# Optimization experiments

Hardware: AMD Instinct MI355X
Metric: run time of the kernel (lower is better)

Reference implementation:

```python
import jax, jax.numpy as jnp
import numpy as np

T, N, C, L, H, NA, NL = 32, 64, 64, 64, 256, 16, 128


def _gru_dir(x, wi, wh, bi, bh):
    # x: [Lt, N, H] time-major; PyTorch GRU gate order (r, z, n). Returns [Lt, N, H].
    xi = jnp.einsum('tnh,gh->tng', x, wi) + bi  # precompute input projections [Lt,N,3H]
    def step(h, gi):
        gh = h @ wh.T + bh
        ir, iz, inn = jnp.split(gi, 3, -1)
        hr, hz, hn = jnp.split(gh, 3, -1)
        r = jax.nn.sigmoid(ir + hr)
        z = jax.nn.sigmoid(iz + hz)
        n = jnp.tanh(inn + r * hn)
        hnew = (1.0 - z) * n + z * h
        return hnew, hnew
    h0 = jnp.zeros((x.shape[1], wh.shape[1]), x.dtype)
    _, ys = jax.lax.scan(step, h0, xi)
    return ys


def setup_inputs() -> dict:
    key = jax.random.key(0)
    ks = jax.random.split(key, 32)
    s = 0.05
    p = {}
    p['condition'] = jax.random.normal(ks[0], (T, N, C), jnp.float32)
    p['lines'] = jax.random.randint(ks[1], (N, L), 0, NL)
    p['a_idx'] = jax.random.randint(ks[2], (T, N), 0, NA)
    p['p_idx'] = jax.random.randint(ks[3], (T, N), 0, L)
    p['embed'] = jax.random.normal(ks[4], (NL, H)) * s
    p['aemb'] = jax.random.normal(ks[5], (NA, H)) * s
    p['gru_wi_f'] = jax.random.normal(ks[6], (3 * H, H)) * s
    p['gru_wh_f'] = jax.random.normal(ks[7], (3 * H, H)) * s
    p['gru_bi_f'] = jax.random.normal(ks[8], (3 * H,)) * s
    p['gru_bh_f'] = jax.random.normal(ks[9], (3 * H,)) * s
    p['gru_wi_b'] = jax.random.normal(ks[10], (3 * H, H)) * s
    p['gru_wh_b'] = jax.random.normal(ks[11], (3 * H, H)) * s
    p['gru_bi_b'] = jax.random.normal(ks[12], (3 * H,)) * s
    p['gru_bh_b'] = jax.random.normal(ks[13], (3 * H,)) * s
    p['f_w1'] = jax.random.normal(ks[14], (H, C + H)) * s
    p['f_b1'] = jax.random.normal(ks[15], (H,)) * s
    p['f_w2'] = jax.random.normal(ks[16], (H, H)) * s
    p['f_b2'] = jax.random.normal(ks[17], (H,)) * s
    p['cell_wi'] = jax.random.normal(ks[18], (3 * H, H)) * s
    p['cell_wh'] = jax.random.normal(ks[19], (3 * H, H)) * s
    p['cell_bi'] = jax.random.normal(ks[20], (3 * H,)) * s
    p['cell_bh'] = jax.random.normal(ks[21], (3 * H,)) * s
    p['critic_w'] = jax.random.normal(ks[22], (1, H)) * s
    p['critic_b'] = jax.random.normal(ks[23], (1,)) * s
    p['pointer_w'] = jax.random.normal(ks[24], (L, H)) * s
    p['pointer_b'] = jax.random.normal(ks[25], (L,)) * s
    p['actor_w'] = jax.random.normal(ks[26], (NA, H)) * s
    p['actor_b'] = jax.random.normal(ks[27], (NA,)) * s
    p['query_w'] = jax.random.normal(ks[28], (H, H)) * s
    p['query_b'] = jax.random.normal(ks[29], (H,)) * s
    return p


def reference(condition, lines, a_idx, p_idx, embed, aemb,
              gru_wi_f, gru_wh_f, gru_bi_f, gru_bh_f,
              gru_wi_b, gru_wh_b, gru_bi_b, gru_bh_b,
              f_w1, f_b1, f_w2, f_b2,
              cell_wi, cell_wh, cell_bi, cell_bh,
              critic_w, critic_b, pointer_w, pointer_b,
              actor_w, actor_b, query_w, query_b):
    Tn, Nn = a_idx.shape
    Ln = lines.shape[1]
    Hd = embed.shape[1]
    M = embed[lines]                           # [N,L,H]
    x = jnp.transpose(M, (1, 0, 2))            # [L,N,H] time-major
    # torch.roll(x, shifts=i): rolled[i, j] = x[(j - i) % L]
    idx = (jnp.arange(Ln)[None, :] - jnp.arange(Ln)[:, None]) % Ln
    rolled = x[idx]                            # [L_roll, L_time, N, H]
    def bigru(seq):
        f = _gru_dir(seq, gru_wi_f, gru_wh_f, gru_bi_f, gru_bh_f)
        b = _gru_dir(seq[::-1], gru_wi_b, gru_wh_b, gru_bi_b, gru_bh_b)[::-1]
        return jnp.concatenate([f, b], -1)     # [L_time,N,2H]
    K1 = jax.vmap(bigru)(rolled)               # [L,L,N,2H]
    K = K1.reshape(Ln, Ln, Nn, 2, Hd).transpose(2, 0, 1, 3, 4).reshape(Nn, Ln, 2 * Ln, Hd)
    # A[t-1] for t=0 is hx.a == 0 (fresh episode, zero hidden state)
    a_prev = jnp.concatenate([jnp.zeros((1, Nn), a_idx.dtype), a_idx[:-1]], 0)
    rng_n = jnp.arange(Nn)
    def step(h, inp):
        cond_t, ap_t, p_t, a_t = inp
        obs = jnp.concatenate([cond_t, aemb[ap_t]], -1)
        xf = jax.nn.relu(obs @ f_w1.T + f_b1)
        xf = jax.nn.relu(xf @ f_w2.T + f_b2)
        gi = xf @ cell_wi.T + cell_bi
        gh = h @ cell_wh.T + cell_bh
        ir, iz, inn = jnp.split(gi, 3, -1)
        hr, hz, hn = jnp.split(gh, 3, -1)
        r = jax.nn.sigmoid(ir + hr)
        z = jax.nn.sigmoid(iz + hz)
        n = jnp.tanh(inn + r * hn)
        h = (1.0 - z) * n + z * h
        p_probs = jax.nn.softmax(h @ pointer_w.T + pointer_b, -1)
        q = h @ query_w.T + query_b
        k = K[rng_n, p_t]                      # gather: [N, 2L, H]
        l = jnp.einsum('nkh,nh->nk', k, q)
        zz = jnp.einsum('nk,nkh->nh', l, k)
        a_probs = jax.nn.softmax(zz @ actor_w.T + actor_b, -1)
        v = h @ critic_w.T + critic_b
        out = jnp.concatenate([a_t[:, None].astype(h.dtype), p_t[:, None].astype(h.dtype),
                               v, h, a_probs, p_probs], -1)
        return h, out
    h0 = jnp.zeros((Nn, Hd), condition.dtype)
    _, hxs = jax.lax.scan(step, h0, (condition, a_prev, p_idx, a_idx))
    return hxs  # packed RecurrentState: [T, N, 1+1+1+H+na+L]
```

## Files before the change

### kernel.cpp

```cpp
#include <hip/hip_runtime.h>
#include <hip/hip_bf16.h>
#include <cstddef>
#include <cstdint>

typedef __bf16 bf16;
typedef bf16 bf16x8 __attribute__((ext_vector_type(8)));
typedef float f32x4 __attribute__((ext_vector_type(4)));

#define DEV static __device__ __forceinline__

DEV f32x4 mfma_bf16(bf16x8 a, bf16x8 b, f32x4 c) {
  return __builtin_amdgcn_mfma_f32_16x16x32_bf16(a, b, c, 0, 0, 0);
}
DEV f32x4 mfma_fp8(long a, long b, f32x4 c) {
  return __builtin_amdgcn_mfma_f32_16x16x32_fp8_fp8(a, b, c, 0, 0, 0);
}

DEV float sigmoid_f(float x) { return 1.0f / (1.0f + __expf(-x)); }
DEV float tanh_f(float x) {
  float ax = fabsf(x);
  float e = __expf(-2.0f * ax);
  float t = 1.0f - 2.0f * e / (1.0f + e);
  return copysignf(t, x);
}
DEV unsigned char fp8_of(float x) {
  return (unsigned char)(__builtin_amdgcn_cvt_pk_fp8_f32(x, x, 0, false) & 0xFF);
}

static constexpr int H_ = 256;

static constexpr int o_embed = 0;
static constexpr int o_aemb = 32768;
static constexpr int o_wi_f = 36864;
static constexpr int o_wh_f = 233472;
static constexpr int o_bi_f = 430080;
static constexpr int o_bh_f = 430848;
static constexpr int o_wi_b = 431616;
static constexpr int o_wh_b = 628224;
static constexpr int o_bi_b = 824832;
static constexpr int o_bh_b = 825600;
static constexpr int o_f_w1 = 826368;
static constexpr int o_f_b1 = 908288;
static constexpr int o_f_w2 = 908544;
static constexpr int o_f_b2 = 974080;
static constexpr int o_cell_wi = 974336;
static constexpr int o_cell_wh = 1170944;
static constexpr int o_cell_bi = 1367552;
static constexpr int o_cell_bh = 1368320;
static constexpr int o_critic_w = 1369088;
static constexpr int o_critic_b = 1369344;
static constexpr int o_pointer_w = 1369360;
static constexpr int o_pointer_b = 1385744;
static constexpr int o_actor_w = 1385808;
static constexpr int o_actor_b = 1389904;
static constexpr int o_query_w = 1389920;
static constexpr int o_query_b = 1455456;
static constexpr int CW_TOTAL = 1455712;
static constexpr int WH8_TOTAL = 393216;
static constexpr int PREP_TOTAL = CW_TOTAL + WH8_TOTAL;
static constexpr int PREP_WGS = (PREP_TOTAL + 2047) / 2048;

static constexpr size_t XI_OFF = 0;
static constexpr size_t XI_BYTES = 2ull * 4096 * 768 * 2;
static constexpr size_t K1_OFF = XI_OFF + XI_BYTES;
static constexpr size_t K1_BYTES = 64ull * 32 * 128 * 256;
static constexpr size_t GI_OFF = K1_OFF + K1_BYTES;
static constexpr size_t GI_BYTES = 32ull * 64 * 768 * 4;
static constexpr size_t HD_OFF = GI_OFF + GI_BYTES;
static constexpr size_t HD_BYTES = 32ull * 64 * 256 * 4;
static constexpr size_t SLOT_OFF = HD_OFF + HD_BYTES;
static constexpr size_t SLOT_BYTES = 64ull * 64 * 4;
static constexpr size_t FLG_OFF = SLOT_OFF + SLOT_BYTES;
static constexpr size_t FLG_BYTES = 256;
static constexpr size_t WL_OFF = FLG_OFF + FLG_BYTES;
static constexpr size_t WL_BYTES = 8448;
static constexpr size_t CW_OFF = WL_OFF + WL_BYTES;
static constexpr size_t CW_BYTES = (size_t)CW_TOTAL * 2;
static constexpr size_t WH8_OFF = ((CW_OFF + CW_BYTES + 255) / 256) * 256;

static constexpr int XI_DIR_BYTES = 4096 * 768 * 2;
static constexpr int XI_U_BYTES = 64 * 768 * 2;

struct PrepArgs {
  const void* src[26];
  int off[26];
  int cnt[26];
};

__global__ __launch_bounds__(256)
void k_prep(PrepArgs pa, const uint32_t* __restrict__ cond, const uint32_t* __restrict__ emb,
            const void* __restrict__ whf_src, const void* __restrict__ whb_src,
            const int* __restrict__ p_idx, int* __restrict__ flags,
            bf16* __restrict__ cw, unsigned char* __restrict__ wh8,
            int* __restrict__ slot_map, int* __restrict__ wl) {
  int bx = blockIdx.x;
  int tid = threadIdx.x;
  __shared__ int votes[256];

  int c1 = 0;
  {
    uint32_t w0 = emb[tid * 2], w1 = emb[tid * 2 + 1];
    int e0 = (int)((w0 >> 7) & 0xFF), e1 = (int)((w1 >> 7) & 0xFF);
    c1 += (e0 >= 96 && e0 <= 130) ? 1 : 0;
    c1 += (e1 >= 96 && e1 <= 130) ? 1 : 0;
  }
  votes[tid] = c1;
  __syncthreads();
  __shared__ int f32w_s;
  if (tid == 0) {
    int s = 0;
    for (int i = 0; i < 256; i++) s += votes[i];
    f32w_s = (s < 256) ? 1 : 0;
  }
  __syncthreads();
  bool f32w = f32w_s != 0;

  if (bx == 0) {
    __syncthreads();
    int c0 = 0;
    {
      uint32_t w0 = cond[tid * 2], w1 = cond[tid * 2 + 1];
      int e0 = (int)((w0 >> 7) & 0xFF), e1 = (int)((w1 >> 7) & 0xFF);
      c0 += (e0 >= 96 && e0 <= 130) ? 1 : 0;
      c0 += (e1 >= 96 && e1 <= 130) ? 1 : 0;
    }
    votes[tid] = c0;
    __syncthreads();
    if (tid == 0) {
      int s = 0;
      for (int i = 0; i < 256; i++) s += votes[i];
      flags[0] = (s < 256) ? 1 : 0;
      flags[1] = f32w ? 1 : 0;
    }
  }

  if (bx < PREP_WGS) {
    int gidx = bx * 2048 + tid;
    for (int e = 0; e < 8; e++, gidx += 256) {
      if (gidx >= PREP_TOTAL) break;
      if (gidx < CW_TOTAL) {
        int rem = gidx, s = 0;
        while (s < 26 && rem >= pa.cnt[s]) { rem -= pa.cnt[s]; s++; }
        if (s < 26) {
          float v = f32w ? ((const float*)pa.src[s])[rem]
                         : (float)((const bf16*)pa.src[s])[rem];
          cw[pa.off[s] + rem] = (bf16)v;
        }
      } else {
        int i = gidx - CW_TOTAL;
        const void* src = (i < 196608) ? whf_src : whb_src;
        int k = (i < 196608) ? i : i - 196608;
        float v = f32w ? ((const float*)src)[k] : (float)((const bf16*)src)[k];
        wh8[i] = fp8_of(v);
      }
    }
    return;
  }

  __shared__ int pbuf[2048];
  __shared__ signed char sm[4096];
  __shared__ unsigned short entL[8 * 512];
  __shared__ int cntL[8];
  for (int i = tid; i < 2048; i += 256) pbuf[i] = p_idx[i];
  for (int i = tid; i < 4096; i += 256) sm[i] = -1;
  __syncthreads();
  if (tid < 64) {
    int n = tid, cnt = 0;
    for (int t = 0; t < 32; t++) {
      int p = pbuf[t * 64 + n];
      if (sm[n * 64 + p] < 0) sm[n * 64 + p] = (signed char)(cnt++);
    }
  }
  __syncthreads();
  for (int i = tid; i < 4096; i += 256) slot_map[i] = (int)sm[i];
  if (tid < 8) {
    int xcd = tid, cnt = 0;
    for (int roll = xcd * 8; roll < xcd * 8 + 8; roll++)
      for (int n = 0; n < 64; n++)
        if (sm[n * 64 + roll] >= 0) entL[xcd * 512 + (cnt++)] = (unsigned short)(n | (roll << 8));
    unsigned short pad = (unsigned short)((xcd * 8) << 8);
    while (cnt & 15) entL[xcd * 512 + (cnt++)] = pad;
    cntL[xcd] = cnt;
  }
  __syncthreads();
  if (tid < 8) wl[tid] = cntL[tid] >> 4;
  unsigned short* we = (unsigned short*)((char*)wl + 64);
  for (int i = tid; i < 8 * 512; i += 256) we[i] = entL[i];
}

__global__ __launch_bounds__(256)
void k_xi_gi(const int* __restrict__ lines, const bf16* __restrict__ cw,
             const void* __restrict__ cond_raw, const int* __restrict__ flags,
             const int* __restrict__ a_idx, bf16* __restrict__ xi,
             float* __restrict__ gi) {
  int bx = blockIdx.x;
  int tid = threadIdx.x;
  int w = tid >> 6, l = tid & 63, quad = l >> 4, l15 = l & 15;
  __shared__ __attribute__((aligned(16))) bf16 s_a[32 * 328];
  __shared__ __attribute__((aligned(16))) bf16 s_b[32 * 264];

  if (bx < 256) {
    int dir = bx & 1, rb = bx >> 1;
    const bf16* embed = cw + o_embed;
    const bf16* wi = cw + (dir ? o_wi_b : o_wi_f);
    const bf16* bi = cw + (dir ? o_bi_b : o_bi_f);
    bf16* xs = s_a;
    {
      int row = tid >> 3, seg = tid & 7;
      int grow = rb * 32 + row;
      int u = grow >> 6, n = grow & 63;
      int line = lines[n * 64 + u];
      const bf16* src = embed + (size_t)line * H_ + seg * 32;
      bf16* dst = xs + row * 264 + seg * 32;
#pragma unroll
      for (int e = 0; e < 4; e++) *(bf16x8*)(dst + e * 8) = *(const bf16x8*)(src + e * 8);
    }
    __syncthreads();
    f32x4 acc[2][12];
#pragma unroll
    for (int mt = 0; mt < 2; mt++)
#pragma unroll
      for (int nt = 0; nt < 12; nt++) acc[mt][nt] = f32x4{0.f, 0.f, 0.f, 0.f};
#pragma unroll
    for (int ks = 0; ks < 8; ks++) {
      int koff = ks * 32 + quad * 8;
      bf16x8 a0 = *(const bf16x8*)(xs + l15 * 264 + koff);
      bf16x8 a1 = *(const bf16x8*)(xs + (l15 + 16) * 264 + koff);
#pragma unroll
      for (int nt = 0; nt < 12; nt++) {
        int g = (w * 12 + nt) * 16 + l15;
        bf16x8 b = *(const bf16x8*)(wi + (size_t)g * H_ + koff);
        acc[0][nt] = mfma_bf16(a0, b, acc[0][nt]);
        acc[1][nt] = mfma_bf16(a1, b, acc[1][nt]);
      }
    }
    size_t base = (size_t)dir * 4096 * 768;
#pragma unroll
    for (int nt = 0; nt < 12; nt++) {
      int g = (w * 12 + nt) * 16 + l15;
      float bias = (float)bi[g];
#pragma unroll
      for (int mt = 0; mt < 2; mt++)
#pragma unroll
        for (int r = 0; r < 4; r++) {
          int m = mt * 16 + quad * 4 + r;
          xi[base + (size_t)(rb * 32 + m) * 768 + g] = (bf16)(acc[mt][nt][r] + bias);
        }
    }
    return;
  }

  int rb = bx - 256;
  const bf16* aemb = cw + o_aemb;
  const bf16* f_w1 = cw + o_f_w1;
  const bf16* f_b1 = cw + o_f_b1;
  const bf16* f_w2 = cw + o_f_w2;
  const bf16* f_b2 = cw + o_f_b2;
  const bf16* cell_wi = cw + o_cell_wi;
  const bf16* cell_bi = cw + o_cell_bi;
  bool cf32 = flags[0] != 0;
  bf16* obs = s_a;
  bf16* xf1 = s_b;

  for (int e = tid; e < 32 * 320; e += 256) {
    int row = e / 320, col = e - row * 320;
    int grow = rb * 32 + row;
    int t = grow >> 6, n = grow & 63;
    float v;
    if (col < 64) {
      v = cf32 ? ((const float*)cond_raw)[(size_t)grow * 64 + col]
               : (float)((const bf16*)cond_raw)[(size_t)grow * 64 + col];
    } else {
      int ap = (t == 0) ? 0 : a_idx[(t - 1) * 64 + n];
      v = (float)aemb[ap * 256 + (col - 64)];
    }
    obs[row * 328 + col] = (bf16)v;
  }
  __syncthreads();
  {
    f32x4 acc[2][4];
#pragma unroll
    for (int mt = 0; mt < 2; mt++)
#pragma unroll
      for (int nt = 0; nt < 4; nt++) acc[mt][nt] = f32x4{0.f, 0.f, 0.f, 0.f};
#pragma unroll
    for (int ks = 0; ks < 10; ks++) {
      int koff = ks * 32 + quad * 8;
      bf16x8 a0 = *(const bf16x8*)(obs + l15 * 328 + koff);
      bf16x8 a1 = *(const bf16x8*)(obs + (l15 + 16) * 328 + koff);
#pragma unroll
      for (int nt = 0; nt < 4; nt++) {
        int g = (w * 4 + nt) * 16 + l15;
        bf16x8 b = *(const bf16x8*)(f_w1 + (size_t)g * 320 + koff);
        acc[0][nt] = mfma_bf16(a0, b, acc[0][nt]);
        acc[1][nt] = mfma_bf16(a1, b, acc[1][nt]);
      }
    }
#pragma unroll
    for (int nt = 0; nt < 4; nt++) {
      int g = (w * 4 + nt) * 16 + l15;
      float bias = (float)f_b1[g];
#pragma unroll
      for (int mt = 0; mt < 2; mt++)
#pragma unroll
        for (int r = 0; r < 4; r++) {
          int m = mt * 16 + quad * 4 + r;
          xf1[m * 264 + g] = (bf16)fmaxf(acc[mt][nt][r] + bias, 0.f);
        }
    }
  }
  __syncthreads();
  bf16* xf2 = obs;
  {
    f32x4 acc[2][4];
#pragma unroll
    for (int mt = 0; mt < 2; mt++)
#pragma unroll
      for (int nt = 0; nt < 4; nt++) acc[mt][nt] = f32x4{0.f, 0.f, 0.f, 0.f};
#pragma unroll
    for (int ks = 0; ks < 8; ks++) {
      int koff = ks * 32 + quad * 8;
      bf16x8 a0 = *(const bf16x8*)(xf1 + l15 * 264 + koff);
      bf16x8 a1 = *(const bf16x8*)(xf1 + (l15 + 16) * 264 + koff);
#pragma unroll
      for (int nt = 0; nt < 4; nt++) {
        int g = (w * 4 + nt) * 16 + l15;
        bf16x8 b = *(const bf16x8*)(f_w2 + (size_t)g * 256 + koff);
        acc[0][nt] = mfma_bf16(a0, b, acc[0][nt]);
        acc[1][nt] = mfma_bf16(a1, b, acc[1][nt]);
      }
    }
#pragma unroll
    for (int nt = 0; nt < 4; nt++) {
      int g = (w * 4 + nt) * 16 + l15;
      float bias = (float)f_b2[g];
#pragma unroll
      for (int mt = 0; mt < 2; mt++)
#pragma unroll
        for (int r = 0; r < 4; r++) {
          int m = mt * 16 + quad * 4 + r;
          xf2[m * 264 + g] = (bf16)fmaxf(acc[mt][nt][r] + bias, 0.f);
        }
    }
  }
  __syncthreads();
  {
    f32x4 acc[2][12];
#pragma unroll
    for (int mt = 0; mt < 2; mt++)
#pragma unroll
      for (int nt = 0; nt < 12; nt++) acc[mt][nt] = f32x4{0.f, 0.f, 0.f, 0.f};
#pragma unroll
    for (int ks = 0; ks < 8; ks++) {
      int koff = ks * 32 + quad * 8;
      bf16x8 a0 = *(const bf16x8*)(xf2 + l15 * 264 + koff);
      bf16x8 a1 = *(const bf16x8*)(xf2 + (l15 + 16) * 264 + koff);
#pragma unroll
      for (int nt = 0; nt < 12; nt++) {
        int g = (w * 12 + nt) * 16 + l15;
        bf16x8 b = *(const bf16x8*)(cell_wi + (size_t)g * 256 + koff);
        acc[0][nt] = mfma_bf16(a0, b, acc[0][nt]);
        acc[1][nt] = mfma_bf16(a1, b, acc[1][nt]);
      }
    }
#pragma unroll
    for (int nt = 0; nt < 12; nt++) {
      int g = (w * 12 + nt) * 16 + l15;
      float bias = (float)cell_bi[g];
#pragma unroll
      for (int mt = 0; mt < 2; mt++)
#pragma unroll
        for (int r = 0; r < 4; r++) {
          int m = mt * 16 + quad * 4 + r;
          gi[(size_t)(rb * 32 + m) * 768 + g] = acc[mt][nt][r] + bias;
        }
    }
  }
}

__global__ __launch_bounds__(1024, 4)
void k_main(const bf16* __restrict__ cw, const unsigned char* __restrict__ wh8,
            const bf16* __restrict__ xi, const int* __restrict__ slot_map,
            const int* __restrict__ wl, const float* __restrict__ gi,
            unsigned char* __restrict__ K1c, float* __restrict__ hdec) {
  int bx = blockIdx.x;
  int tid = threadIdx.x;
  int w = tid >> 6, l = tid & 63, quad = l >> 4, l15 = l & 15;
  int c = w * 16 + l15;
  __shared__ __attribute__((aligned(16))) unsigned char smem[2][16 * 264 * 2];

  if (bx < 512) {
    int xcd = bx & 7, dir = (bx >> 3) & 1, slot = bx >> 4;
    if (slot >= wl[xcd]) return;
    const unsigned short* we = (const unsigned short*)((const char*)wl + 64) + xcd * 512 + slot * 16;
    const unsigned char* whd = wh8 + (size_t)dir * 196608;
    const bf16* bh = cw + (dir ? o_bh_b : o_bh_f);

    unsigned char (*hb)[16 * 264 * 2] = smem;
    for (int idx = tid; idx < 16 * 264; idx += 1024) hb[0][idx] = 0;

    long bfr[3][8];
#pragma unroll
    for (int g = 0; g < 3; g++) {
      const unsigned char* bp = whd + (size_t)(g * 256 + c) * 256 + quad * 8;
#pragma unroll
      for (int ks = 0; ks < 8; ks++) bfr[g][ks] = *(const long*)(bp + ks * 32);
    }

    int xoff[4];
    uint32_t slice[4];
    bool valid[4];
#pragma unroll
    for (int r = 0; r < 4; r++) {
      int e = we[quad * 4 + r];
      int roll = e >> 8, n = e & 255;
      int u0 = dir ? ((63 - roll) & 63) : ((64 - roll) & 63);
      xoff[r] = u0 * XI_U_BYTES + n * 1536 + c * 2;
      int ks = slot_map[n * 64 + roll];
      valid[r] = ks >= 0;
      slice[r] = (uint32_t)((n * 32 + (ks < 0 ? 0 : ks)) * 32768);
    }
    int ustep = dir ? -XI_U_BYTES : XI_U_BYTES;
    int jbase = dir ? (63 * 2 + 1) * 256 : 0;
    int jstep = dir ? -512 : 512;

    float hreg[4] = {0.f, 0.f, 0.f, 0.f};
    float bhv[3];
#pragma unroll
    for (int g = 0; g < 3; g++) bhv[g] = (float)bh[g * 256 + c];

    const char* xid = (const char*)xi + (size_t)dir * XI_DIR_BYTES;
    __syncthreads();

    int cur = 0;
    for (int t = 0; t < 64; t++) {
      float xiv[3][4];
#pragma unroll
      for (int r = 0; r < 4; r++) {
        const bf16* xp = (const bf16*)(xid + xoff[r]);
        xiv[0][r] = (float)xp[0];
        xiv[1][r] = (float)xp[256];
        xiv[2][r] = (float)xp[512];
        xoff[r] += ustep;
        if (xoff[r] >= XI_DIR_BYTES) xoff[r] -= XI_DIR_BYTES;
        if (xoff[r] < 0) xoff[r] += XI_DIR_BYTES;
      }

      f32x4 accA[3], accB[3];
#pragma unroll
      for (int g = 0; g < 3; g++) {
        accA[g] = f32x4{0.f, 0.f, 0.f, 0.f};
        accB[g] = f32x4{0.f, 0.f, 0.f, 0.f};
      }
#pragma unroll
      for (int ks = 0; ks < 4; ks++) {
        long a0 = *(const long*)(hb[cur] + l15 * 264 + ks * 32 + quad * 8);
        long a1 = *(const long*)(hb[cur] + l15 * 264 + (ks + 4) * 32 + quad * 8);
#pragma unroll
        for (int g = 0; g < 3; g++) {
          accA[g] = mfma_fp8(a0, bfr[g][ks], accA[g]);
          accB[g] = mfma_fp8(a1, bfr[g][ks + 4], accB[g]);
        }
      }

      int nxt = cur ^ 1;
#pragma unroll
      for (int r = 0; r < 4; r++) {
        float rg = sigmoid_f(xiv[0][r] + accA[0][r] + accB[0][r] + bhv[0]);
        float zg = sigmoid_f(xiv[1][r] + accA[1][r] + accB[1][r] + bhv[1]);
        float ng = tanh_f(xiv[2][r] + rg * (accA[2][r] + accB[2][r] + bhv[2]));
        hreg[r] = (1.f - zg) * ng + zg * hreg[r];
        unsigned char hb8 = fp8_of(hreg[r]);
        hb[nxt][(quad * 4 + r) * 264 + c] = hb8;
        if (valid[r]) K1c[(size_t)slice[r] + jbase + c] = hb8;
      }
      jbase += jstep;
      __syncthreads();
      cur = nxt;
    }
    return;
  }

  int nq = bx - 512;
  const bf16* wh = cw + o_cell_wh;
  const bf16* bh = cw + o_cell_bh;
  bf16 (*hb)[16 * 264] = (bf16(*)[16 * 264])smem;
  for (int idx = tid; idx < 16 * 264; idx += 1024) hb[0][idx] = (bf16)0.f;

  float hreg[4] = {0.f, 0.f, 0.f, 0.f};
  float bhv[3];
  const bf16* bp[3];
#pragma unroll
  for (int g = 0; g < 3; g++) {
    int grow = g * 256 + c;
    bhv[g] = (float)bh[grow];
    bp[g] = wh + (size_t)grow * 256 + quad * 8;
  }
  __syncthreads();

  int cur = 0;
  for (int t = 0; t < 32; t++) {
    const float* gr = gi + ((size_t)t * 64 + nq * 16) * 768;
    float giv[3][4];
#pragma unroll
    for (int r = 0; r < 4; r++)
#pragma unroll
      for (int g = 0; g < 3; g++)
        giv[g][r] = gr[(quad * 4 + r) * 768 + g * 256 + c];

    f32x4 acc[3];
#pragma unroll
    for (int g = 0; g < 3; g++) acc[g] = f32x4{0.f, 0.f, 0.f, 0.f};
#pragma unroll
    for (int ks = 0; ks < 8; ks++) {
      int ko = ks * 32 + quad * 8;
      bf16x8 a0 = *(const bf16x8*)(hb[cur] + l15 * 264 + ko);
#pragma unroll
      for (int g = 0; g < 3; g++) {
        bf16x8 b = *(const bf16x8*)(bp[g] + ks * 32);
        acc[g] = mfma_bf16(a0, b, acc[g]);
      }
    }
    int nxt = cur ^ 1;
#pragma unroll
    for (int r = 0; r < 4; r++) {
      float rg = sigmoid_f(giv[0][r] + acc[0][r] + bhv[0]);
      float zg = sigmoid_f(giv[1][r] + acc[1][r] + bhv[1]);
      float ng = tanh_f(giv[2][r] + rg * (acc[2][r] + bhv[2]));
      float hnew = (1.f - zg) * ng + zg * hreg[r];
      hreg[r] = hnew;
      hb[nxt][(quad * 4 + r) * 264 + c] = (bf16)hnew;
      hdec[((size_t)t * 64 + nq * 16 + quad * 4 + r) * 256 + c] = hnew;
    }
    __syncthreads();
    cur = nxt;
  }
}

__global__ __launch_bounds__(256)
void k_post(const float* __restrict__ hdec, const unsigned char* __restrict__ K1c,
            const int* __restrict__ slot_map, const int* __restrict__ flags,
            const int* __restrict__ a_idx, const int* __restrict__ p_idx,
            const bf16* __restrict__ cw, void* __restrict__ out_raw) {
  int bx = blockIdx.x;
  int tid = threadIdx.x;
  int w = tid >> 6, l = tid & 63, quad = l >> 4, l15 = l & 15;
  __shared__ __attribute__((aligned(16))) unsigned char sraw[38032];
  bool f32o = flags[1] != 0;

  if (bx < 64) {
    int rb = bx;
    const bf16* pointer_w = cw + o_pointer_w;
    const bf16* pointer_b = cw + o_pointer_b;
    const bf16* critic_w = cw + o_critic_w;
    const bf16* critic_b = cw + o_critic_b;
    bf16* hsb = (bf16*)sraw;
    float* pls = (float*)(sraw + 16896);
    float* vred = (float*)(sraw + 16896 + 8448);

    for (int idx = tid; idx < 32 * 256; idx += 256) {
      int row = idx >> 8, col = idx & 255;
      hsb[row * 264 + col] = (bf16)hdec[(size_t)(rb * 32 + row) * 256 + col];
    }
    __syncthreads();

    {
      f32x4 acc[2];
      acc[0] = f32x4{0.f, 0.f, 0.f, 0.f};
      acc[1] = f32x4{0.f, 0.f, 0.f, 0.f};
      int g = w * 16 + l15;
#pragma unroll
      for (int ks = 0; ks < 8; ks++) {
        int koff = ks * 32 + quad * 8;
        bf16x8 a0 = *(const bf16x8*)(hsb + l15 * 264 + koff);
        bf16x8 a1 = *(const bf16x8*)(hsb + (l15 + 16) * 264 + koff);
        bf16x8 b = *(const bf16x8*)(pointer_w + (size_t)g * 256 + koff);
        acc[0] = mfma_bf16(a0, b, acc[0]);
        acc[1] = mfma_bf16(a1, b, acc[1]);
      }
      float bias = (float)pointer_b[g];
#pragma unroll
      for (int mt = 0; mt < 2; mt++)
#pragma unroll
        for (int r = 0; r < 4; r++) {
          int m = mt * 16 + quad * 4 + r;
          pls[m * 66 + g] = acc[mt][r] + bias;
        }
    }
    {
      int row = tid >> 3, seg = tid & 7;
      float acc = 0.f;
#pragma unroll
      for (int k = 0; k < 32; k++)
        acc += (float)hsb[row * 264 + seg * 32 + k] * (float)critic_w[seg * 32 + k];
      vred[row * 8 + seg] = acc;
    }
    __syncthreads();

    if (tid < 32) {
      float mx = -1e30f;
      for (int k = 0; k < 64; k++) mx = fmaxf(mx, pls[tid * 66 + k]);
      float sm = 0.f;
      for (int k = 0; k < 64; k++) {
        float e = __expf(pls[tid * 66 + k] - mx);
        pls[tid * 66 + k] = e;
        sm += e;
      }
      float inv = 1.f / sm;
      for (int k = 0; k < 64; k++) pls[tid * 66 + k] *= inv;
      float v = (float)critic_b[0];
      for (int s = 0; s < 8; s++) v += vred[tid * 8 + s];
      vred[tid * 8] = v;
    }
    __syncthreads();

    if (f32o) {
      float* ob = (float*)out_raw;
      if (tid < 32) {
        int grow = rb * 32 + tid;
        ob[(size_t)grow * 339 + 0] = (float)a_idx[grow];
        ob[(size_t)grow * 339 + 1] = (float)p_idx[grow];
        ob[(size_t)grow * 339 + 2] = vred[tid * 8];
      }
      for (int idx = tid; idx < 32 * 256; idx += 256) {
        int row = idx >> 8, col = idx & 255;
        int grow = rb * 32 + row;
        ob[(size_t)grow * 339 + 3 + col] = hdec[(size_t)grow * 256 + col];
      }
      for (int idx = tid; idx < 32 * 64; idx += 256) {
        int row = idx >> 6, col = idx & 63;
        ob[(size_t)(rb * 32 + row) * 339 + 275 + col] = pls[row * 66 + col];
      }
    } else {
      bf16* ob = (bf16*)out_raw;
      if (tid < 32) {
        int grow = rb * 32 + tid;
        ob[(size_t)grow * 339 + 0] = (bf16)(float)a_idx[grow];
        ob[(size_t)grow * 339 + 1] = (bf16)(float)p_idx[grow];
        ob[(size_t)grow * 339 + 2] = (bf16)vred[tid * 8];
      }
      for (int idx = tid; idx < 32 * 256; idx += 256) {
        int row = idx >> 8, col = idx & 255;
        int grow = rb * 32 + row;
        ob[(size_t)grow * 339 + 3 + col] = (bf16)hdec[(size_t)grow * 256 + col];
      }
      for (int idx = tid; idx < 32 * 64; idx += 256) {
        int row = idx >> 6, col = idx & 63;
        ob[(size_t)(rb * 32 + row) * 339 + 275 + col] = (bf16)pls[row * 66 + col];
      }
    }
    return;
  }

  int tn = bx - 64;
  int t = tn >> 6, n = tn & 63;
  const bf16* actor_w = cw + o_actor_w;
  const bf16* actor_b = cw + o_actor_b;
  const bf16* query_w = cw + o_query_w;
  const bf16* query_b = cw + o_query_b;

  unsigned char* ksb = sraw;
  float* hs = (float*)(sraw + 33792);
  float* qs = (float*)(sraw + 33792 + 1024);
  float* ls = (float*)(sraw + 33792 + 2048);
  float* sA = (float*)(sraw + 33792 + 3072);
  float* al = (float*)(sraw + 33792 + 4096);

  hs[tid] = hdec[((size_t)t * 64 + n) * 256 + tid];
  int p = p_idx[t * 64 + n];
  int slot = slot_map[n * 64 + p];
  {
    const uint32_t* kg = (const uint32_t*)(K1c + ((size_t)n * 32 + slot) * 32768);
#pragma unroll
    for (int e = 0; e < 8; e++) {
      int flat = (e * 256 + tid) * 16;
      int kk = flat >> 8, col = flat & 255;
      uint32_t w0 = kg[(flat >> 2) + 0], w1 = kg[(flat >> 2) + 1];
      uint32_t w2 = kg[(flat >> 2) + 2], w3 = kg[(flat >> 2) + 3];
      uint32_t* d0 = (uint32_t*)(ksb + kk * 264 + col);
      d0[0] = w0; d0[1] = w1; d0[2] = w2; d0[3] = w3;
    }
  }
  __syncthreads();

  {
    float acc = (float)query_b[tid];
    const bf16* qw = query_w + (size_t)tid * 256;
#pragma unroll 4
    for (int k0 = 0; k0 < 256; k0 += 8) {
      bf16x8 wv = *(const bf16x8*)(qw + k0);
#pragma unroll
      for (int e = 0; e < 8; e++) acc += (float)wv[e] * hs[k0 + e];
    }
    qs[tid] = acc;
  }
  __syncthreads();

  {
    int kk = tid & 127, hc = tid >> 7;
    const uint32_t* kr = (const uint32_t*)(ksb + kk * 264 + hc * 128);
    const float* qr = qs + hc * 128;
    float acc = 0.f;
#pragma unroll 8
    for (int u = 0; u < 32; u++) {
      uint32_t b4 = kr[u];
      acc += __builtin_amdgcn_cvt_f32_fp8(b4, 0) * qr[u * 4 + 0];
      acc += __builtin_amdgcn_cvt_f32_fp8(b4, 1) * qr[u * 4 + 1];
      acc += __builtin_amdgcn_cvt_f32_fp8(b4, 2) * qr[u * 4 + 2];
      acc += __builtin_amdgcn_cvt_f32_fp8(b4, 3) * qr[u * 4 + 3];
    }
    ls[tid] = acc;
  }
  __syncthreads();
  if (tid < 128) ls[tid] += ls[tid + 128];
  __syncthreads();

  float zzv;
  {
    const unsigned char* kc = ksb + (tid & ~3);
    int sh = (tid & 3) * 8;
    float acc = 0.f;
#pragma unroll 8
    for (int kk = 0; kk < 128; kk++) {
      uint32_t d = *(const uint32_t*)(kc + kk * 264);
      acc += ls[kk] * __builtin_amdgcn_cvt_f32_fp8((int)(d >> sh), 0);
    }
    zzv = acc;
  }
  __syncthreads();
  qs[tid] = zzv;
  __syncthreads();

  {
    int a = tid >> 4, e = tid & 15;
    const bf16* aw = actor_w + (size_t)a * 256 + e * 16;
    const float* zr = qs + e * 16;
    float acc = 0.f;
#pragma unroll
    for (int hh = 0; hh < 16; hh++) acc += (float)aw[hh] * zr[hh];
    sA[tid] = acc;
  }
  __syncthreads();
  if (tid < 16) {
    float lg = (float)actor_b[tid];
#pragma unroll
    for (int e = 0; e < 16; e++) lg += sA[tid * 16 + e];
    float mx = lg;
#pragma unroll
    for (int m = 8; m > 0; m >>= 1) mx = fmaxf(mx, __shfl_xor(mx, m, 16));
    float ex = __expf(lg - mx);
    float sm = ex;
#pragma unroll
    for (int m = 8; m > 0; m >>= 1) sm += __shfl_xor(sm, m, 16);
    al[tid] = ex / sm;
  }
  __syncthreads();

  if (tid < 16) {
    size_t off = (size_t)(t * 64 + n) * 339 + 259 + tid;
    if (f32o) ((float*)out_raw)[off] = al[tid];
    else ((bf16*)out_raw)[off] = (bf16)al[tid];
  }
}

extern "C" void kernel_launch(void* const* d_in, const int* in_sizes, int n_in,
                              void* d_out, int out_size, void* d_ws, size_t ws_size,
                              hipStream_t stream) {
  (void)in_sizes; (void)n_in; (void)out_size; (void)ws_size;
  const void* condition = d_in[0];
  const int* lines      = (const int*)d_in[1];
  const int* a_idx      = (const int*)d_in[2];
  const int* p_idx      = (const int*)d_in[3];

  char* ws = (char*)d_ws;
  bf16* xi            = (bf16*)(ws + XI_OFF);
  unsigned char* K1c  = (unsigned char*)(ws + K1_OFF);
  float* gi           = (float*)(ws + GI_OFF);
  float* hdec         = (float*)(ws + HD_OFF);
  int* slot_map       = (int*)(ws + SLOT_OFF);
  int* flags          = (int*)(ws + FLG_OFF);
  int* wl             = (int*)(ws + WL_OFF);
  bf16* cw            = (bf16*)(ws + CW_OFF);
  unsigned char* wh8  = (unsigned char*)(ws + WH8_OFF);

  static const int src_idx[26] = {4, 5, 6, 7, 8, 9, 10, 11, 12, 13, 14, 15, 16,
                                  17, 18, 19, 20, 21, 22, 23, 24, 25, 26, 27, 28, 29};
  static const int offs[26] = {o_embed, o_aemb, o_wi_f, o_wh_f, o_bi_f, o_bh_f,
                               o_wi_b, o_wh_b, o_bi_b, o_bh_b, o_f_w1, o_f_b1,
                               o_f_w2, o_f_b2, o_cell_wi, o_cell_wh, o_cell_bi,
                               o_cell_bh, o_critic_w, o_critic_b, o_pointer_w,
                               o_pointer_b, o_actor_w, o_actor_b, o_query_w, o_query_b};
  static const int cnts[26] = {32768, 4096, 196608, 196608, 768, 768,
                               196608, 196608, 768, 768, 81920, 256,
                               65536, 256, 196608, 196608, 768,
                               768, 256, 1, 16384, 64, 4096, 16, 65536, 256};
  PrepArgs pa;
  for (int i = 0; i < 26; i++) {
    pa.src[i] = d_in[src_idx[i]];
    pa.off[i] = offs[i];
    pa.cnt[i] = cnts[i];
  }

  k_prep<<<PREP_WGS + 1, 256, 0, stream>>>(pa, (const uint32_t*)condition,
                                           (const uint32_t*)d_in[4], d_in[7], d_in[11],
                                           p_idx, flags, cw, wh8, slot_map, wl);
  k_xi_gi<<<320, 256, 0, stream>>>(lines, cw, condition, flags, a_idx, xi, gi);
  k_main<<<516, 1024, 0, stream>>>(cw, wh8, xi, slot_map, wl, gi, K1c, hdec);
  k_post<<<2112, 256, 0, stream>>>(hdec, K1c, slot_map, flags, a_idx, p_idx, cw, d_out);
}
```

Before: 453.8 us.

## Halve rows per GRU workgroup, double grid, stream weights and coalesce K1 stores

The bidirectional GRU encoder now packs 8 sequences per workgroup instead of 16, so twice as many workgroups run with launch bounds raised to allow 8 waves per SIMD. The fp8 recurrent weights are reloaded from global or cache on each step instead of being held in registers, which cuts register pressure to fit the higher occupancy. K1 stores become coalesced 4-byte copies from shared memory after the barrier instead of scattered byte stores. In exchange, each MFMA tile carries duplicated rows, there is more weight-load traffic per step, and the mapping logic is more complex.

```diff
diff --git a/kernel.cpp b/kernel.cpp
--- a/kernel.cpp
+++ b/kernel.cpp
@@ -78,9 +78,6 @@
 static constexpr size_t CW_BYTES = (size_t)CW_TOTAL * 2;
 static constexpr size_t WH8_OFF = ((CW_OFF + CW_BYTES + 255) / 256) * 256;
 
-static constexpr int XI_DIR_BYTES = 4096 * 768 * 2;
-static constexpr int XI_U_BYTES = 64 * 768 * 2;
-
 struct PrepArgs {
   const void* src[26];
   int off[26];
@@ -179,11 +176,11 @@
       for (int n = 0; n < 64; n++)
         if (sm[n * 64 + roll] >= 0) entL[xcd * 512 + (cnt++)] = (unsigned short)(n | (roll << 8));
     unsigned short pad = (unsigned short)((xcd * 8) << 8);
-    while (cnt & 15) entL[xcd * 512 + (cnt++)] = pad;
+    while (cnt & 7) entL[xcd * 512 + (cnt++)] = pad;
     cntL[xcd] = cnt;
   }
   __syncthreads();
-  if (tid < 8) wl[tid] = cntL[tid] >> 4;
+  if (tid < 8) wl[tid] = cntL[tid] >> 3;
   unsigned short* we = (unsigned short*)((char*)wl + 64);
   for (int i = tid; i < 8 * 512; i += 256) we[i] = entL[i];
 }
@@ -378,7 +375,7 @@
   }
 }
 
-__global__ __launch_bounds__(1024, 4)
+__global__ __launch_bounds__(1024, 8)
 void k_main(const bf16* __restrict__ cw, const unsigned char* __restrict__ wh8,
             const bf16* __restrict__ xi, const int* __restrict__ slot_map,
             const int* __restrict__ wl, const float* __restrict__ gi,
@@ -389,99 +386,86 @@
   int c = w * 16 + l15;
   __shared__ __attribute__((aligned(16))) unsigned char smem[2][16 * 264 * 2];
 
-  if (bx < 512) {
+  if (bx < 1024) {
     int xcd = bx & 7, dir = (bx >> 3) & 1, slot = bx >> 4;
     if (slot >= wl[xcd]) return;
-    const unsigned short* we = (const unsigned short*)((const char*)wl + 64) + xcd * 512 + slot * 16;
+    const unsigned short* we =
+        (const unsigned short*)((const char*)wl + 64) + xcd * 512 + slot * 8;
     const unsigned char* whd = wh8 + (size_t)dir * 196608;
     const bf16* bh = cw + (dir ? o_bh_b : o_bh_f);
 
     unsigned char (*hb)[16 * 264 * 2] = smem;
     for (int idx = tid; idx < 16 * 264; idx += 1024) hb[0][idx] = 0;
 
-    long bfr[3][8];
-#pragma unroll
-    for (int g = 0; g < 3; g++) {
-      const unsigned char* bp = whd + (size_t)(g * 256 + c) * 256 + quad * 8;
-#pragma unroll
-      for (int ks = 0; ks < 8; ks++) bfr[g][ks] = *(const long*)(bp + ks * 32);
-    }
-
-    int xoff[4];
-    uint32_t slice[4];
-    bool valid[4];
+    int rollv[4], nbase[4];
 #pragma unroll
     for (int r = 0; r < 4; r++) {
-      int e = we[quad * 4 + r];
-      int roll = e >> 8, n = e & 255;
-      int u0 = dir ? ((63 - roll) & 63) : ((64 - roll) & 63);
-      xoff[r] = u0 * XI_U_BYTES + n * 1536 + c * 2;
-      int ks = slot_map[n * 64 + roll];
-      valid[r] = ks >= 0;
-      slice[r] = (uint32_t)((n * 32 + (ks < 0 ? 0 : ks)) * 32768);
-    }
-    int ustep = dir ? -XI_U_BYTES : XI_U_BYTES;
-    int jbase = dir ? (63 * 2 + 1) * 256 : 0;
-    int jstep = dir ? -512 : 512;
+      int e = we[(quad * 4 + r) & 7];
+      rollv[r] = e >> 8;
+      nbase[r] = (e & 255) * 768;
+    }
+    int crow = tid >> 6, cseg = tid & 63;
+    int ec = we[crow & 7];
+    int n_c = ec & 255, roll_c = ec >> 8;
+    int kslot = slot_map[n_c * 64 + roll_c];
+    unsigned char* dstb = K1c + ((size_t)n_c * 32 + (kslot < 0 ? 0 : kslot)) * 32768 + cseg * 4;
 
     float hreg[4] = {0.f, 0.f, 0.f, 0.f};
     float bhv[3];
-#pragma unroll
-    for (int g = 0; g < 3; g++) bhv[g] = (float)bh[g * 256 + c];
-
-    const char* xid = (const char*)xi + (size_t)dir * XI_DIR_BYTES;
+    const unsigned char* bp[3];
+#pragma unroll
+    for (int g = 0; g < 3; g++) {
+      int grow = g * 256 + c;
+      bhv[g] = (float)bh[grow];
+      bp[g] = whd + (size_t)grow * 256 + quad * 8;
+    }
+    const bf16* xid = xi + (size_t)dir * 4096 * 768;
     __syncthreads();
 
     int cur = 0;
     for (int t = 0; t < 64; t++) {
+      int j = dir ? (63 - t) : t;
       float xiv[3][4];
 #pragma unroll
       for (int r = 0; r < 4; r++) {
-        const bf16* xp = (const bf16*)(xid + xoff[r]);
-        xiv[0][r] = (float)xp[0];
-        xiv[1][r] = (float)xp[256];
-        xiv[2][r] = (float)xp[512];
-        xoff[r] += ustep;
-        if (xoff[r] >= XI_DIR_BYTES) xoff[r] -= XI_DIR_BYTES;
-        if (xoff[r] < 0) xoff[r] += XI_DIR_BYTES;
-      }
-
-      f32x4 accA[3], accB[3];
-#pragma unroll
-      for (int g = 0; g < 3; g++) {
-        accA[g] = f32x4{0.f, 0.f, 0.f, 0.f};
-        accB[g] = f32x4{0.f, 0.f, 0.f, 0.f};
-      }
-#pragma unroll
-      for (int ks = 0; ks < 4; ks++) {
-        long a0 = *(const long*)(hb[cur] + l15 * 264 + ks * 32 + quad * 8);
-        long a1 = *(const long*)(hb[cur] + l15 * 264 + (ks + 4) * 32 + quad * 8);
+        int u = dir ? ((63 - t - rollv[r]) & 63) : ((t - rollv[r]) & 63);
+        const bf16* xr = xid + u * 49152 + nbase[r] + c;
+#pragma unroll
+        for (int g = 0; g < 3; g++) xiv[g][r] = (float)xr[g * 256];
+      }
+      f32x4 acc[3];
+#pragma unroll
+      for (int g = 0; g < 3; g++) acc[g] = f32x4{0.f, 0.f, 0.f, 0.f};
+#pragma unroll
+      for (int ks = 0; ks < 8; ks++) {
+        int ko = ks * 32 + quad * 8;
+        long a0 = *(const long*)(hb[cur] + l15 * 264 + ko);
 #pragma unroll
         for (int g = 0; g < 3; g++) {
-          accA[g] = mfma_fp8(a0, bfr[g][ks], accA[g]);
-          accB[g] = mfma_fp8(a1, bfr[g][ks + 4], accB[g]);
+          long b = *(const long*)(bp[g] + ks * 32);
+          acc[g] = mfma_fp8(a0, b, acc[g]);
         }
       }
-
       int nxt = cur ^ 1;
 #pragma unroll
       for (int r = 0; r < 4; r++) {
-        float rg = sigmoid_f(xiv[0][r] + accA[0][r] + accB[0][r] + bhv[0]);
-        float zg = sigmoid_f(xiv[1][r] + accA[1][r] + accB[1][r] + bhv[1]);
-        float ng = tanh_f(xiv[2][r] + rg * (accA[2][r] + accB[2][r] + bhv[2]));
+        float rg = sigmoid_f(xiv[0][r] + acc[0][r] + bhv[0]);
+        float zg = sigmoid_f(xiv[1][r] + acc[1][r] + bhv[1]);
+        float ng = tanh_f(xiv[2][r] + rg * (acc[2][r] + bhv[2]));
         hreg[r] = (1.f - zg) * ng + zg * hreg[r];
-        unsigned char hb8 = fp8_of(hreg[r]);
-        hb[nxt][(quad * 4 + r) * 264 + c] = hb8;
-        if (valid[r]) K1c[(size_t)slice[r] + jbase + c] = hb8;
-      }
-      jbase += jstep;
+        hb[nxt][(quad * 4 + r) * 264 + c] = fp8_of(hreg[r]);
+      }
       __syncthreads();
+      if (kslot >= 0) {
+        *(uint32_t*)(dstb + (size_t)(j * 2 + dir) * 256) =
+            *(const uint32_t*)(hb[nxt] + crow * 264 + cseg * 4);
+      }
       cur = nxt;
     }
     return;
   }
 
-  int nq = bx - 512;
+  int nq = bx - 1024;
   const bf16* wh = cw + o_cell_wh;
   const bf16* bh = cw + o_cell_bh;
   bf16 (*hb)[16 * 264] = (bf16(*)[16 * 264])smem;
@@ -805,6 +789,6 @@
                                            (const uint32_t*)d_in[4], d_in[7], d_in[11],
                                            p_idx, flags, cw, wh8, slot_map, wl);
   k_xi_gi<<<320, 256, 0, stream>>>(lines, cw, condition, flags, a_idx, xi, gi);
-  k_main<<<516, 1024, 0, stream>>>(cw, wh8, xi, slot_map, wl, gi, K1c, hdec);
+  k_main<<<1028, 1024, 0, stream>>>(cw, wh8, xi, slot_map, wl, gi, K1c, hdec);
   k_post<<<2112, 256, 0, stream>>>(hdec, K1c, slot_map, flags, a_idx, p_idx, cw, d_out);
 }
```

Result: slower. 956.9 us (+110.9%).
